# Kernel tuning notes

Measured on AMD Instinct MI355X. Metric: run time of the kernel, lower is better.

The kernel has to match this reference:

```python
import jax, jax.numpy as jnp
import numpy as np

HEADS = 8
DIM_HEAD = 64
QUERY_DIM = 512
CONTEXT_DIM = 768
INNER = HEADS * DIM_HEAD  # 512
SCALE = DIM_HEAD ** -0.5


def setup_inputs() -> dict:
    key = jax.random.key(0)
    ks = jax.random.split(key, 7)
    B, N, M = 4, 2048, 2048
    x = jax.random.normal(ks[0], (B, N, QUERY_DIM), dtype=jnp.float32)
    context = jax.random.normal(ks[1], (B, M, CONTEXT_DIM), dtype=jnp.float32)
    # torch Linear weights: [out_features, in_features], y = x @ W.T
    s = 0.02
    Wq = jax.random.normal(ks[2], (INNER, QUERY_DIM), dtype=jnp.float32) * s
    Wk = jax.random.normal(ks[3], (INNER, CONTEXT_DIM), dtype=jnp.float32) * s
    Wv = jax.random.normal(ks[4], (INNER, CONTEXT_DIM), dtype=jnp.float32) * s
    Wo = jax.random.normal(ks[5], (QUERY_DIM, INNER), dtype=jnp.float32) * s
    bo = jax.random.normal(ks[6], (QUERY_DIM,), dtype=jnp.float32) * s
    return {"x": x, "context": context, "Wq": Wq, "Wk": Wk, "Wv": Wv, "Wo": Wo, "bo": bo}


def reference(x, context, Wq, Wk, Wv, Wo, bo):
    b, n, _ = x.shape
    m = context.shape[1]
    h, d = HEADS, DIM_HEAD
    # Projections (bias=False for q/k/v)
    q = jnp.einsum('bnc,ec->bne', x, Wq)        # [b, n, inner]
    k = jnp.einsum('bmc,ec->bme', context, Wk)  # [b, m, inner]
    v = jnp.einsum('bmc,ec->bme', context, Wv)
    # Split heads
    q = q.reshape(b, n, h, d)
    k = k.reshape(b, m, h, d)
    v = v.reshape(b, m, h, d)
    # Scores in fp32 (original casts q,k to float), scaled by dim_head**-0.5
    sim = jnp.einsum('bihd,bjhd->bhij', q.astype(jnp.float32), k.astype(jnp.float32)) * SCALE
    attn = jax.nn.softmax(sim, axis=-1).astype(v.dtype)
    out = jnp.einsum('bhij,bjhd->bihd', attn, v).reshape(b, n, h * d)
    # Output projection with bias (dropout=0 -> identity)
    return jnp.einsum('bne,oe->bno', out, Wo) + bo
```

## Files before the change

kernel.cpp:

```cpp
#include <hip/hip_runtime.h>
#include <hip/hip_bf16.h>
#include <math.h>


typedef __bf16 bf16x8 __attribute__((ext_vector_type(8)));
typedef __bf16 bf16x4 __attribute__((ext_vector_type(4)));
typedef short s16x4 __attribute__((ext_vector_type(4)));
typedef float f32x4 __attribute__((ext_vector_type(4)));

#define QSCALE 0.18033688011112042f

__device__ __forceinline__ f32x4 mfma32(bf16x8 a, bf16x8 b, f32x4 c) {
  return __builtin_amdgcn_mfma_f32_16x16x32_bf16(a, b, c, 0, 0, 0);
}
__device__ __forceinline__ f32x4 mfma16(s16x4 a, s16x4 b, f32x4 c) {
  return __builtin_amdgcn_mfma_f32_16x16x16bf16_1k(a, b, c, 0, 0, 0);
}

__global__ __launch_bounds__(256) void cast_all(
    const float* __restrict__ x, const float* __restrict__ ctx,
    const float* __restrict__ wq, const float* __restrict__ wk,
    const float* __restrict__ wv, const float* __restrict__ wo,
    __bf16* __restrict__ xb, __bf16* __restrict__ cb,
    __bf16* __restrict__ wqb, __bf16* __restrict__ wkb,
    __bf16* __restrict__ wvb, __bf16* __restrict__ wob) {
  const int B0 = 1048576;
  const int B1 = 2621440;
  const int B2 = 2686976;
  const int B3 = 2785280;
  const int B4 = 2883584;
  const int B5 = 2949120;
  for (int i = blockIdx.x * blockDim.x + threadIdx.x; i < B5;
       i += gridDim.x * blockDim.x) {
    const float* s;
    __bf16* d;
    int off;
    if (i < B0)      { s = x;   d = xb;  off = i; }
    else if (i < B1) { s = ctx; d = cb;  off = i - B0; }
    else if (i < B2) { s = wq;  d = wqb; off = i - B1; }
    else if (i < B3) { s = wk;  d = wkb; off = i - B2; }
    else if (i < B4) { s = wv;  d = wvb; off = i - B3; }
    else             { s = wo;  d = wob; off = i - B4; }
    float4 f = ((const float4*)s)[off];
    union { __bf16 b[4]; ushort4 u; } cv;
    cv.b[0] = (__bf16)f.x; cv.b[1] = (__bf16)f.y;
    cv.b[2] = (__bf16)f.z; cv.b[3] = (__bf16)f.w;
    ((ushort4*)d)[off] = cv.u;
  }
}

template <int MODE>
__device__ __forceinline__ void gemm_body(
    const __bf16* __restrict__ A, const __bf16* __restrict__ B,
    __bf16* __restrict__ Cout, int Kd, float scale, int m0, int n0,
    __bf16 (*As)[40], __bf16 (*Bs)[40]) {
  const int t = threadIdx.x;
  const int w = t >> 6;
  const int lane = t & 63;
  const int ln = lane & 15;
  const int qd = lane >> 4;
  const int wm = (w >> 1) * 64;
  const int wn = (w & 1) * 64;

  f32x4 zero4 = {0.f, 0.f, 0.f, 0.f};
  f32x4 acc[4][4];
#pragma unroll
  for (int i = 0; i < 4; ++i)
#pragma unroll
    for (int j = 0; j < 4; ++j) acc[i][j] = zero4;

  const int r = t >> 1;
  const int c0 = (t & 1) * 16;
  const __bf16* gA = A + (size_t)(m0 + r) * Kd + c0;
  const __bf16* gB = B + (size_t)(n0 + r) * Kd + c0;

  for (int kc = 0; kc < Kd; kc += 32) {
    uint4 a0 = *(const uint4*)(gA + kc);
    uint4 a1 = *(const uint4*)(gA + kc + 8);
    uint4 b0 = *(const uint4*)(gB + kc);
    uint4 b1 = *(const uint4*)(gB + kc + 8);
    __syncthreads();
    *(uint4*)&As[r][c0] = a0;
    *(uint4*)&As[r][c0 + 8] = a1;
    *(uint4*)&Bs[r][c0] = b0;
    *(uint4*)&Bs[r][c0 + 8] = b1;
    __syncthreads();
    bf16x8 af[4], bfr[4];
#pragma unroll
    for (int i = 0; i < 4; ++i) {
      af[i] = *(const bf16x8*)&As[wm + i * 16 + ln][qd * 8];
      bfr[i] = *(const bf16x8*)&Bs[wn + i * 16 + ln][qd * 8];
    }
#pragma unroll
    for (int i = 0; i < 4; ++i)
#pragma unroll
      for (int j = 0; j < 4; ++j) {
        if (MODE == 1)
          acc[i][j] = mfma32(af[i], bfr[j], acc[i][j]);
        else
          acc[i][j] = mfma32(bfr[j], af[i], acc[i][j]);
      }
  }

#pragma unroll
  for (int i = 0; i < 4; ++i)
#pragma unroll
    for (int j = 0; j < 4; ++j) {
      if (MODE == 0) {
        const int gm = m0 + wm + i * 16 + ln;
        const int gn0 = n0 + wn + j * 16 + qd * 4;
        const int bb = gm >> 11, tok = gm & 2047;
        const int hh = gn0 >> 6, dd0 = gn0 & 63;
        bf16x4 v;
#pragma unroll
        for (int rg = 0; rg < 4; ++rg) v[rg] = (__bf16)(acc[i][j][rg] * scale);
        *(bf16x4*)(Cout + (((size_t)bb * 8 + hh) * 2048 + tok) * 64 + dd0) = v;
      } else {
        const int gm0 = m0 + wm + i * 16 + qd * 4;
        const int gn = n0 + wn + j * 16 + ln;
        const int bb = gm0 >> 11;
        const int tokbase = (gm0 & 2047) & ~31;
        const int up = qd * 8 + (i & 1) * 4;
        const int hh = gn >> 6, dd = gn & 63;
        bf16x4 v;
#pragma unroll
        for (int rg = 0; rg < 4; ++rg) v[rg] = (__bf16)acc[i][j][rg];
        *(bf16x4*)(Cout + (((size_t)bb * 8 + hh) * 64 + dd) * 2048 + tokbase +
                   up) = v;
      }
    }
}

__global__ __launch_bounds__(256, 3) void proj_qkv(
    const __bf16* __restrict__ xb, const __bf16* __restrict__ cb,
    const __bf16* __restrict__ Wq, const __bf16* __restrict__ Wk,
    const __bf16* __restrict__ Wv, __bf16* __restrict__ Qw,
    __bf16* __restrict__ Kw, __bf16* __restrict__ Vtw) {
  __shared__ __bf16 As[128][40];
  __shared__ __bf16 Bs[128][40];
  const int m0 = blockIdx.x * 128;
  const int job = blockIdx.y >> 2;
  const int n0 = (blockIdx.y & 3) * 128;
  if (job == 0)
    gemm_body<0>(xb, Wq, Qw, 512, QSCALE, m0, n0, As, Bs);
  else if (job == 1)
    gemm_body<0>(cb, Wk, Kw, 768, 1.0f, m0, n0, As, Bs);
  else
    gemm_body<1>(cb, Wv, Vtw, 768, 1.0f, m0, n0, As, Bs);
}

__global__ __launch_bounds__(256) void gemm_out(
    const __bf16* __restrict__ O0, const __bf16* __restrict__ O1,
    const float* __restrict__ lbuf,
    const __bf16* __restrict__ B,
    float* __restrict__ C, const float* __restrict__ bias) {
  const int m0 = blockIdx.x * 64;
  const int n0 = blockIdx.y * 128;
  const int t = threadIdx.x;
  const int w = t >> 6;
  const int lane = t & 63;
  const int ln = lane & 15;
  const int qd = lane >> 4;
  const int wm = (w >> 1) * 32;
  const int wn = (w & 1) * 64;

  __shared__ __bf16 As[64][40];
  __shared__ __bf16 Bs[128][40];

  f32x4 zero4 = {0.f, 0.f, 0.f, 0.f};
  f32x4 acc[2][4];
#pragma unroll
  for (int i = 0; i < 2; ++i)
#pragma unroll
    for (int j = 0; j < 4; ++j) acc[i][j] = zero4;

  const int ra = t >> 2, ca = (t & 3) * 8;
  const int rb = t >> 1, cb = (t & 1) * 16;
  const int gm_s = m0 + ra;
  const int bidx = gm_s >> 11, tok_s = gm_s & 2047;
  const size_t aoff = (size_t)gm_s * 512 + ca;
  const __bf16* gB = B + (size_t)(n0 + rb) * 512 + cb;

  float inv[8];
#pragma unroll
  for (int hh = 0; hh < 8; ++hh) {
    const float l0 = lbuf[((size_t)bidx * 8 + hh) * 2048 + tok_s];
    const float l1 = lbuf[65536 + ((size_t)bidx * 8 + hh) * 2048 + tok_s];
    inv[hh] = 1.0f / (l0 + l1);
  }

#pragma unroll
  for (int kc = 0; kc < 512; kc += 32) {
    const float iv = inv[kc >> 6];
    union { bf16x8 v; uint4 u; } u0, u1, rr;
    u0.u = *(const uint4*)(O0 + aoff + kc);
    u1.u = *(const uint4*)(O1 + aoff + kc);
    uint4 b0 = *(const uint4*)(gB + kc);
    uint4 b1 = *(const uint4*)(gB + kc + 8);
#pragma unroll
    for (int e = 0; e < 8; ++e)
      rr.v[e] = (__bf16)(((float)u0.v[e] + (float)u1.v[e]) * iv);
    __syncthreads();
    *(uint4*)&As[ra][ca] = rr.u;
    *(uint4*)&Bs[rb][cb] = b0;
    *(uint4*)&Bs[rb][cb + 8] = b1;
    __syncthreads();
    bf16x8 af[2], bfr[4];
#pragma unroll
    for (int i = 0; i < 2; ++i)
      af[i] = *(const bf16x8*)&As[wm + i * 16 + ln][qd * 8];
#pragma unroll
    for (int j = 0; j < 4; ++j)
      bfr[j] = *(const bf16x8*)&Bs[wn + j * 16 + ln][qd * 8];
#pragma unroll
    for (int i = 0; i < 2; ++i)
#pragma unroll
      for (int j = 0; j < 4; ++j)
        acc[i][j] = mfma32(bfr[j], af[i], acc[i][j]);
  }

#pragma unroll
  for (int i = 0; i < 2; ++i)
#pragma unroll
    for (int j = 0; j < 4; ++j) {
      const int gm = m0 + wm + i * 16 + ln;
      const int gn0 = n0 + wn + j * 16 + qd * 4;
      f32x4 bi = *(const f32x4*)&bias[gn0];
      f32x4 v = acc[i][j] + bi;
      *(f32x4*)&C[(size_t)gm * 512 + gn0] = v;
    }
}

__global__ __launch_bounds__(256, 4) void attn_kernel(
    const __bf16* __restrict__ Q,
    const __bf16* __restrict__ K,
    const __bf16* __restrict__ Vt,
    __bf16* __restrict__ Oh,
    float* __restrict__ lbuf) {
  const int S = 2048;
  const int qt = blockIdx.x;
  const int bh = blockIdx.y;
  const int sp = blockIdx.z;
  const int b = bh >> 3, h = bh & 7;
  const int t = threadIdx.x;
  const int w = t >> 6;
  const int lane = t & 63;
  const int ln = lane & 15;
  const int qd = lane >> 4;

  __shared__ __align__(16) __bf16 Ks[128][72];
  __shared__ __align__(16) __bf16 Vts[64][136];

  bf16x8 bq[2][2];
  {
    const __bf16* qb =
        Q + ((size_t)bh * S + qt * 128 + w * 32 + ln) * 64 + qd * 8;
#pragma unroll
    for (int mt = 0; mt < 2; ++mt)
#pragma unroll
      for (int kst = 0; kst < 2; ++kst)
        bq[mt][kst] = *(const bf16x8*)(qb + mt * 1024 + kst * 32);
  }

  f32x4 zero4 = {0.f, 0.f, 0.f, 0.f};
  f32x4 o[2][4];
#pragma unroll
  for (int mt = 0; mt < 2; ++mt)
#pragma unroll
    for (int i = 0; i < 4; ++i) o[mt][i] = zero4;
  float lrow[2] = {0.f, 0.f};

  const int kr = t >> 1, kc = (t & 1) * 32;
  const int vd = t >> 2, vc = (t & 3) * 32;
  const int kt0 = sp * 8;

  for (int kt = kt0; kt < kt0 + 8; ++kt) {
    const uint4* gK =
        (const uint4*)(K + ((size_t)bh * S + kt * 128 + kr) * 64 + kc);
    const uint4* gV =
        (const uint4*)(Vt + ((size_t)bh * 64 + vd) * S + kt * 128 + vc);
    uint4 kv0 = gK[0], kv1 = gK[1], kv2 = gK[2], kv3 = gK[3];
    uint4 vv0 = gV[0], vv1 = gV[1], vv2 = gV[2], vv3 = gV[3];
    __syncthreads();
    {
      uint4* dK = (uint4*)&Ks[kr][kc];
      dK[0] = kv0; dK[1] = kv1; dK[2] = kv2; dK[3] = kv3;
      uint4* dV = (uint4*)&Vts[vd][vc];
      dV[0] = vv0; dV[1] = vv1; dV[2] = vv2; dV[3] = vv3;
    }
    __syncthreads();

#pragma unroll
    for (int c = 0; c < 4; ++c) {
      bf16x8 av[4];
#pragma unroll
      for (int i = 0; i < 4; ++i)
        av[i] = *(const bf16x8*)&Vts[i * 16 + ln][c * 32 + qd * 8];

      f32x4 s[2][2];
      s[0][0] = zero4; s[0][1] = zero4; s[1][0] = zero4; s[1][1] = zero4;
#pragma unroll
      for (int e = 0; e < 2; ++e) {
        const int nt = c * 2 + e;
#pragma unroll
        for (int kst = 0; kst < 2; ++kst) {
          bf16x8 ak = *(const bf16x8*)&Ks[nt * 16 + ln][kst * 32 + qd * 8];
          s[e][0] = mfma32(ak, bq[0][kst], s[e][0]);
          s[e][1] = mfma32(ak, bq[1][kst], s[e][1]);
        }
      }
#pragma unroll
      for (int e = 0; e < 2; ++e)
#pragma unroll
        for (int mt = 0; mt < 2; ++mt) {
          float rs = 0.f;
#pragma unroll
          for (int rg = 0; rg < 4; ++rg) {
            float p = exp2f(s[e][mt][rg]);
            s[e][mt][rg] = p;
            rs += p;
          }
          lrow[mt] += rs;
        }
#pragma unroll
      for (int e = 0; e < 2; ++e) {
        bf16x4 c0, c1;
#pragma unroll
        for (int rg = 0; rg < 4; ++rg) {
          c0[rg] = (__bf16)s[e][0][rg];
          c1[rg] = (__bf16)s[e][1][rg];
        }
        s16x4 p0 = __builtin_bit_cast(s16x4, c0);
        s16x4 p1 = __builtin_bit_cast(s16x4, c1);
#pragma unroll
        for (int i = 0; i < 4; ++i) {
          union { bf16x8 v; bf16x4 hh[2]; } U;
          U.v = av[i];
          s16x4 a = __builtin_bit_cast(s16x4, U.hh[e]);
          o[0][i] = mfma16(a, p0, o[0][i]);
          o[1][i] = mfma16(a, p1, o[1][i]);
        }
      }
    }
  }

  __bf16* Osp = Oh + (size_t)sp * 8192 * 512;
#pragma unroll
  for (int mt = 0; mt < 2; ++mt) {
    float l = lrow[mt];
    l += __shfl_xor(l, 16);
    l += __shfl_xor(l, 32);
    const int tok = qt * 128 + w * 32 + mt * 16 + ln;
    if (qd == 0) lbuf[((size_t)sp * 32 + bh) * 2048 + tok] = l;
#pragma unroll
    for (int i = 0; i < 4; ++i) {
      bf16x4 v;
#pragma unroll
      for (int rg = 0; rg < 4; ++rg) v[rg] = (__bf16)o[mt][i][rg];
      const int col = h * 64 + i * 16 + qd * 4;
      *(bf16x4*)&Osp[((size_t)b * S + tok) * 512 + col] = v;
    }
  }
}

extern "C" void kernel_launch(void* const* d_in, const int* in_sizes, int n_in,
                              void* d_out, int out_size, void* d_ws,
                              size_t ws_size, hipStream_t stream) {
  const float* x = (const float*)d_in[0];
  const float* ctx = (const float*)d_in[1];
  const float* Wq = (const float*)d_in[2];
  const float* Wk = (const float*)d_in[3];
  const float* Wv = (const float*)d_in[4];
  const float* Wo = (const float*)d_in[5];
  const float* bo = (const float*)d_in[6];

  char* p = (char*)d_ws;
  __bf16* xb = (__bf16*)p;   p += (size_t)8192 * 512 * 2;
  __bf16* cb = (__bf16*)p;   p += (size_t)8192 * 768 * 2;
  __bf16* wqb = (__bf16*)p;  p += (size_t)512 * 512 * 2;
  __bf16* wkb = (__bf16*)p;  p += (size_t)512 * 768 * 2;
  __bf16* wvb = (__bf16*)p;  p += (size_t)512 * 768 * 2;
  __bf16* wob = (__bf16*)p;  p += (size_t)512 * 512 * 2;
  __bf16* Qw = (__bf16*)p;   p += (size_t)8192 * 512 * 2;
  __bf16* Kw = (__bf16*)p;   p += (size_t)8192 * 512 * 2;
  __bf16* Vtw = (__bf16*)p;  p += (size_t)8192 * 512 * 2;
  __bf16* Oh = (__bf16*)p;   p += (size_t)2 * 8192 * 512 * 2;
  float* lbuf = (float*)p;   p += (size_t)2 * 32 * 2048 * 4;

  cast_all<<<2880, 256, 0, stream>>>(x, ctx, Wq, Wk, Wv, Wo, xb, cb, wqb, wkb,
                                     wvb, wob);

  dim3 gp(64, 12);
  proj_qkv<<<gp, 256, 0, stream>>>(xb, cb, wqb, wkb, wvb, Qw, Kw, Vtw);

  dim3 ga(16, 32, 2);
  attn_kernel<<<ga, 256, 0, stream>>>(Qw, Kw, Vtw, Oh, lbuf);

  dim3 go(128, 4);
  gemm_out<<<go, 256, 0, stream>>>(Oh, Oh + (size_t)8192 * 512, lbuf, wob,
                                   (float*)d_out, bo);
}
```

Measured before the change: 206.4 us.

## Double-buffer GEMMs with direct global-to-LDS loads and compute row sums via MFMA

The projection and output GEMMs switch to global_load_lds direct copies into a double-buffered, k-chunk-major shared layout, dropping one barrier per k step and overlapping the next tile's load with MFMA work. The output GEMM also prefetches and normalises the next A tile in registers. The attention kernel computes softmax row sums with an extra MFMA against a ones vector instead of VALU adds and shuffles, and uses the raw exp2 builtin. The V^T layout is changed to plain token order with a new LDS pitch and narrower reads. Risks include LDS bank conflicts in the unpadded layout and async-load ordering relying on a single barrier.

```diff
diff --git a/kernel.cpp b/kernel.cpp
--- a/kernel.cpp
+++ b/kernel.cpp
@@ -10,11 +10,23 @@
 
 #define QSCALE 0.18033688011112042f
 
+#if __has_builtin(__builtin_amdgcn_exp2f)
+#define EXP2(x) __builtin_amdgcn_exp2f(x)
+#else
+#define EXP2(x) exp2f(x)
+#endif
+
 __device__ __forceinline__ f32x4 mfma32(bf16x8 a, bf16x8 b, f32x4 c) {
   return __builtin_amdgcn_mfma_f32_16x16x32_bf16(a, b, c, 0, 0, 0);
 }
 __device__ __forceinline__ f32x4 mfma16(s16x4 a, s16x4 b, f32x4 c) {
   return __builtin_amdgcn_mfma_f32_16x16x16bf16_1k(a, b, c, 0, 0, 0);
+}
+
+__device__ __forceinline__ void glds16(const void* g, void* l) {
+  __builtin_amdgcn_global_load_lds(
+      (const __attribute__((address_space(1))) unsigned int*)g,
+      (__attribute__((address_space(3))) unsigned int*)l, 16, 0, 0);
 }
 
 __global__ __launch_bounds__(256) void cast_all(
@@ -53,7 +65,7 @@
 __device__ __forceinline__ void gemm_body(
     const __bf16* __restrict__ A, const __bf16* __restrict__ B,
     __bf16* __restrict__ Cout, int Kd, float scale, int m0, int n0,
-    __bf16 (*As)[40], __bf16 (*Bs)[40]) {
+    __bf16 (*As)[4][128][8], __bf16 (*Bs)[4][128][8]) {
   const int t = threadIdx.x;
   const int w = t >> 6;
   const int lane = t & 63;
@@ -69,27 +81,30 @@
 #pragma unroll
     for (int j = 0; j < 4; ++j) acc[i][j] = zero4;
 
-  const int r = t >> 1;
-  const int c0 = (t & 1) * 16;
-  const __bf16* gA = A + (size_t)(m0 + r) * Kd + c0;
-  const __bf16* gB = B + (size_t)(n0 + r) * Kd + c0;
-
+  const __bf16* gA0 = A + (size_t)(m0 + lane) * Kd + w * 8;
+  const __bf16* gA1 = A + (size_t)(m0 + 64 + lane) * Kd + w * 8;
+  const __bf16* gB0 = B + (size_t)(n0 + lane) * Kd + w * 8;
+  const __bf16* gB1 = B + (size_t)(n0 + 64 + lane) * Kd + w * 8;
+
+  glds16(gA0, &As[0][w][0][0]);
+  glds16(gA1, &As[0][w][64][0]);
+  glds16(gB0, &Bs[0][w][0][0]);
+  glds16(gB1, &Bs[0][w][64][0]);
+
+  int buf = 0;
   for (int kc = 0; kc < Kd; kc += 32) {
-    uint4 a0 = *(const uint4*)(gA + kc);
-    uint4 a1 = *(const uint4*)(gA + kc + 8);
-    uint4 b0 = *(const uint4*)(gB + kc);
-    uint4 b1 = *(const uint4*)(gB + kc + 8);
     __syncthreads();
-    *(uint4*)&As[r][c0] = a0;
-    *(uint4*)&As[r][c0 + 8] = a1;
-    *(uint4*)&Bs[r][c0] = b0;
-    *(uint4*)&Bs[r][c0 + 8] = b1;
-    __syncthreads();
+    if (kc + 32 < Kd) {
+      glds16(gA0 + kc + 32, &As[buf ^ 1][w][0][0]);
+      glds16(gA1 + kc + 32, &As[buf ^ 1][w][64][0]);
+      glds16(gB0 + kc + 32, &Bs[buf ^ 1][w][0][0]);
+      glds16(gB1 + kc + 32, &Bs[buf ^ 1][w][64][0]);
+    }
     bf16x8 af[4], bfr[4];
 #pragma unroll
     for (int i = 0; i < 4; ++i) {
-      af[i] = *(const bf16x8*)&As[wm + i * 16 + ln][qd * 8];
-      bfr[i] = *(const bf16x8*)&Bs[wn + i * 16 + ln][qd * 8];
+      af[i] = *(const bf16x8*)&As[buf][qd][wm + i * 16 + ln][0];
+      bfr[i] = *(const bf16x8*)&Bs[buf][qd][wn + i * 16 + ln][0];
     }
 #pragma unroll
     for (int i = 0; i < 4; ++i)
@@ -100,6 +115,7 @@
         else
           acc[i][j] = mfma32(bfr[j], af[i], acc[i][j]);
       }
+    buf ^= 1;
   }
 
 #pragma unroll
@@ -118,15 +134,12 @@
       } else {
         const int gm0 = m0 + wm + i * 16 + qd * 4;
         const int gn = n0 + wn + j * 16 + ln;
-        const int bb = gm0 >> 11;
-        const int tokbase = (gm0 & 2047) & ~31;
-        const int up = qd * 8 + (i & 1) * 4;
+        const int bb = gm0 >> 11, tok0 = gm0 & 2047;
         const int hh = gn >> 6, dd = gn & 63;
         bf16x4 v;
 #pragma unroll
         for (int rg = 0; rg < 4; ++rg) v[rg] = (__bf16)acc[i][j][rg];
-        *(bf16x4*)(Cout + (((size_t)bb * 8 + hh) * 64 + dd) * 2048 + tokbase +
-                   up) = v;
+        *(bf16x4*)(Cout + (((size_t)bb * 8 + hh) * 64 + dd) * 2048 + tok0) = v;
       }
     }
 }
@@ -136,8 +149,8 @@
     const __bf16* __restrict__ Wq, const __bf16* __restrict__ Wk,
     const __bf16* __restrict__ Wv, __bf16* __restrict__ Qw,
     __bf16* __restrict__ Kw, __bf16* __restrict__ Vtw) {
-  __shared__ __bf16 As[128][40];
-  __shared__ __bf16 Bs[128][40];
+  __shared__ __align__(16) __bf16 As[2][4][128][8];
+  __shared__ __align__(16) __bf16 Bs[2][4][128][8];
   const int m0 = blockIdx.x * 128;
   const int job = blockIdx.y >> 2;
   const int n0 = (blockIdx.y & 3) * 128;
@@ -164,8 +177,8 @@
   const int wm = (w >> 1) * 32;
   const int wn = (w & 1) * 64;
 
-  __shared__ __bf16 As[64][40];
-  __shared__ __bf16 Bs[128][40];
+  __shared__ __align__(16) __bf16 As[2][64][40];
+  __shared__ __align__(16) __bf16 Bs[2][4][128][8];
 
   f32x4 zero4 = {0.f, 0.f, 0.f, 0.f};
   f32x4 acc[2][4];
@@ -175,11 +188,11 @@
     for (int j = 0; j < 4; ++j) acc[i][j] = zero4;
 
   const int ra = t >> 2, ca = (t & 3) * 8;
-  const int rb = t >> 1, cb = (t & 1) * 16;
   const int gm_s = m0 + ra;
   const int bidx = gm_s >> 11, tok_s = gm_s & 2047;
   const size_t aoff = (size_t)gm_s * 512 + ca;
-  const __bf16* gB = B + (size_t)(n0 + rb) * 512 + cb;
+  const __bf16* gB0 = B + (size_t)(n0 + lane) * 512 + w * 8;
+  const __bf16* gB1 = B + (size_t)(n0 + 64 + lane) * 512 + w * 8;
 
   float inv[8];
 #pragma unroll
@@ -189,34 +202,53 @@
     inv[hh] = 1.0f / (l0 + l1);
   }
 
-#pragma unroll
-  for (int kc = 0; kc < 512; kc += 32) {
-    const float iv = inv[kc >> 6];
+  {
     union { bf16x8 v; uint4 u; } u0, u1, rr;
-    u0.u = *(const uint4*)(O0 + aoff + kc);
-    u1.u = *(const uint4*)(O1 + aoff + kc);
-    uint4 b0 = *(const uint4*)(gB + kc);
-    uint4 b1 = *(const uint4*)(gB + kc + 8);
+    u0.u = *(const uint4*)(O0 + aoff);
+    u1.u = *(const uint4*)(O1 + aoff);
+    glds16(gB0, &Bs[0][w][0][0]);
+    glds16(gB1, &Bs[0][w][64][0]);
+    const float iv = inv[0];
 #pragma unroll
     for (int e = 0; e < 8; ++e)
       rr.v[e] = (__bf16)(((float)u0.v[e] + (float)u1.v[e]) * iv);
+    *(uint4*)&As[0][ra][ca] = rr.u;
+  }
+
+  int buf = 0;
+#pragma unroll
+  for (int k = 0; k < 16; ++k) {
     __syncthreads();
-    *(uint4*)&As[ra][ca] = rr.u;
-    *(uint4*)&Bs[rb][cb] = b0;
-    *(uint4*)&Bs[rb][cb + 8] = b1;
-    __syncthreads();
+    uint4 o0n, o1n;
+    if (k < 15) {
+      o0n = *(const uint4*)(O0 + aoff + (k + 1) * 32);
+      o1n = *(const uint4*)(O1 + aoff + (k + 1) * 32);
+      glds16(gB0 + (k + 1) * 32, &Bs[buf ^ 1][w][0][0]);
+      glds16(gB1 + (k + 1) * 32, &Bs[buf ^ 1][w][64][0]);
+    }
     bf16x8 af[2], bfr[4];
 #pragma unroll
     for (int i = 0; i < 2; ++i)
-      af[i] = *(const bf16x8*)&As[wm + i * 16 + ln][qd * 8];
+      af[i] = *(const bf16x8*)&As[buf][wm + i * 16 + ln][qd * 8];
 #pragma unroll
     for (int j = 0; j < 4; ++j)
-      bfr[j] = *(const bf16x8*)&Bs[wn + j * 16 + ln][qd * 8];
+      bfr[j] = *(const bf16x8*)&Bs[buf][qd][wn + j * 16 + ln][0];
 #pragma unroll
     for (int i = 0; i < 2; ++i)
 #pragma unroll
       for (int j = 0; j < 4; ++j)
         acc[i][j] = mfma32(bfr[j], af[i], acc[i][j]);
+    if (k < 15) {
+      union { bf16x8 v; uint4 u; } u0, u1, rr;
+      u0.u = o0n;
+      u1.u = o1n;
+      const float iv = inv[(k + 1) >> 1];
+#pragma unroll
+      for (int e = 0; e < 8; ++e)
+        rr.v[e] = (__bf16)(((float)u0.v[e] + (float)u1.v[e]) * iv);
+      *(uint4*)&As[buf ^ 1][ra][ca] = rr.u;
+    }
+    buf ^= 1;
   }
 
 #pragma unroll
@@ -249,7 +281,7 @@
   const int qd = lane >> 4;
 
   __shared__ __align__(16) __bf16 Ks[128][72];
-  __shared__ __align__(16) __bf16 Vts[64][136];
+  __shared__ __align__(16) __bf16 Vts[64][132];
 
   bf16x8 bq[2][2];
   {
@@ -264,11 +296,14 @@
 
   f32x4 zero4 = {0.f, 0.f, 0.f, 0.f};
   f32x4 o[2][4];
-#pragma unroll
-  for (int mt = 0; mt < 2; ++mt)
+  f32x4 o_l[2];
+#pragma unroll
+  for (int mt = 0; mt < 2; ++mt) {
 #pragma unroll
     for (int i = 0; i < 4; ++i) o[mt][i] = zero4;
-  float lrow[2] = {0.f, 0.f};
+    o_l[mt] = zero4;
+  }
+  const s16x4 ones = {0x3F80, 0x3F80, 0x3F80, 0x3F80};
 
   const int kr = t >> 1, kc = (t & 1) * 32;
   const int vd = t >> 2, vc = (t & 3) * 32;
@@ -285,18 +320,16 @@
     {
       uint4* dK = (uint4*)&Ks[kr][kc];
       dK[0] = kv0; dK[1] = kv1; dK[2] = kv2; dK[3] = kv3;
-      uint4* dV = (uint4*)&Vts[vd][vc];
-      dV[0] = vv0; dV[1] = vv1; dV[2] = vv2; dV[3] = vv3;
+      uint2* dV = (uint2*)&Vts[vd][vc];
+      dV[0] = *(uint2*)&vv0; dV[1] = *((uint2*)&vv0 + 1);
+      dV[2] = *(uint2*)&vv1; dV[3] = *((uint2*)&vv1 + 1);
+      dV[4] = *(uint2*)&vv2; dV[5] = *((uint2*)&vv2 + 1);
+      dV[6] = *(uint2*)&vv3; dV[7] = *((uint2*)&vv3 + 1);
     }
     __syncthreads();
 
 #pragma unroll
     for (int c = 0; c < 4; ++c) {
-      bf16x8 av[4];
-#pragma unroll
-      for (int i = 0; i < 4; ++i)
-        av[i] = *(const bf16x8*)&Vts[i * 16 + ln][c * 32 + qd * 8];
-
       f32x4 s[2][2];
       s[0][0] = zero4; s[0][1] = zero4; s[1][0] = zero4; s[1][1] = zero4;
 #pragma unroll
@@ -312,18 +345,12 @@
 #pragma unroll
       for (int e = 0; e < 2; ++e)
 #pragma unroll
-        for (int mt = 0; mt < 2; ++mt) {
-          float rs = 0.f;
-#pragma unroll
-          for (int rg = 0; rg < 4; ++rg) {
-            float p = exp2f(s[e][mt][rg]);
-            s[e][mt][rg] = p;
-            rs += p;
-          }
-          lrow[mt] += rs;
-        }
+        for (int mt = 0; mt < 2; ++mt)
+#pragma unroll
+          for (int rg = 0; rg < 4; ++rg) s[e][mt][rg] = EXP2(s[e][mt][rg]);
 #pragma unroll
       for (int e = 0; e < 2; ++e) {
+        const int nt = c * 2 + e;
         bf16x4 c0, c1;
 #pragma unroll
         for (int rg = 0; rg < 4; ++rg) {
@@ -332,11 +359,12 @@
         }
         s16x4 p0 = __builtin_bit_cast(s16x4, c0);
         s16x4 p1 = __builtin_bit_cast(s16x4, c1);
+        o_l[0] = mfma16(ones, p0, o_l[0]);
+        o_l[1] = mfma16(ones, p1, o_l[1]);
 #pragma unroll
         for (int i = 0; i < 4; ++i) {
-          union { bf16x8 v; bf16x4 hh[2]; } U;
-          U.v = av[i];
-          s16x4 a = __builtin_bit_cast(s16x4, U.hh[e]);
+          bf16x4 av = *(const bf16x4*)&Vts[i * 16 + ln][nt * 16 + qd * 4];
+          s16x4 a = __builtin_bit_cast(s16x4, av);
           o[0][i] = mfma16(a, p0, o[0][i]);
           o[1][i] = mfma16(a, p1, o[1][i]);
         }
@@ -347,11 +375,8 @@
   __bf16* Osp = Oh + (size_t)sp * 8192 * 512;
 #pragma unroll
   for (int mt = 0; mt < 2; ++mt) {
-    float l = lrow[mt];
-    l += __shfl_xor(l, 16);
-    l += __shfl_xor(l, 32);
     const int tok = qt * 128 + w * 32 + mt * 16 + ln;
-    if (qd == 0) lbuf[((size_t)sp * 32 + bh) * 2048 + tok] = l;
+    if (qd == 0) lbuf[((size_t)sp * 32 + bh) * 2048 + tok] = o_l[mt][0];
 #pragma unroll
     for (int i = 0; i < 4; ++i) {
       bf16x4 v;
```

New measurement: 204.0 us. About the same (-1.2%).

## Shrink GEMM tiles, compute softmax row sums via MFMA, change V layout

Applied to the files above, without the earlier changes.

The QKV projection tile drops from 128x128 to 64x128 and the output GEMM tile from 64x128 to 64x64, which doubles both grids and raises the occupancy hints so more blocks run at once. In the attention kernel, row sums of exp(P) are now accumulated with an extra MFMA against a ones vector rather than scalar adds plus shuffles. V^T is stored in natural token order, and V fragments are read from LDS per step as bf16x4 with a different padding. A raw exp2 builtin is also used. The smaller tiles give up operand reuse per block, and the extra MFMAs and LDS reads add work to the attention inner loop.

```diff
diff --git a/kernel.cpp b/kernel.cpp
--- a/kernel.cpp
+++ b/kernel.cpp
@@ -9,6 +9,12 @@
 typedef float f32x4 __attribute__((ext_vector_type(4)));
 
 #define QSCALE 0.18033688011112042f
+
+#if __has_builtin(__builtin_amdgcn_exp2f)
+#define EXP2(x) __builtin_amdgcn_exp2f(x)
+#else
+#define EXP2(x) exp2f(x)
+#endif
 
 __device__ __forceinline__ f32x4 mfma32(bf16x8 a, bf16x8 b, f32x4 c) {
   return __builtin_amdgcn_mfma_f32_16x16x32_bf16(a, b, c, 0, 0, 0);
@@ -50,7 +56,7 @@
 }
 
 template <int MODE>
-__device__ __forceinline__ void gemm_body(
+__device__ __forceinline__ void gemm_body64(
     const __bf16* __restrict__ A, const __bf16* __restrict__ B,
     __bf16* __restrict__ Cout, int Kd, float scale, int m0, int n0,
     __bf16 (*As)[40], __bf16 (*Bs)[40]) {
@@ -59,40 +65,39 @@
   const int lane = t & 63;
   const int ln = lane & 15;
   const int qd = lane >> 4;
-  const int wm = (w >> 1) * 64;
+  const int wm = (w >> 1) * 32;
   const int wn = (w & 1) * 64;
 
   f32x4 zero4 = {0.f, 0.f, 0.f, 0.f};
-  f32x4 acc[4][4];
-#pragma unroll
-  for (int i = 0; i < 4; ++i)
+  f32x4 acc[2][4];
+#pragma unroll
+  for (int i = 0; i < 2; ++i)
 #pragma unroll
     for (int j = 0; j < 4; ++j) acc[i][j] = zero4;
 
-  const int r = t >> 1;
-  const int c0 = (t & 1) * 16;
-  const __bf16* gA = A + (size_t)(m0 + r) * Kd + c0;
-  const __bf16* gB = B + (size_t)(n0 + r) * Kd + c0;
+  const int ra = t >> 2, ca = (t & 3) * 8;
+  const int rb = t >> 1, cbx = (t & 1) * 16;
+  const __bf16* gA = A + (size_t)(m0 + ra) * Kd + ca;
+  const __bf16* gB = B + (size_t)(n0 + rb) * Kd + cbx;
 
   for (int kc = 0; kc < Kd; kc += 32) {
     uint4 a0 = *(const uint4*)(gA + kc);
-    uint4 a1 = *(const uint4*)(gA + kc + 8);
     uint4 b0 = *(const uint4*)(gB + kc);
     uint4 b1 = *(const uint4*)(gB + kc + 8);
     __syncthreads();
-    *(uint4*)&As[r][c0] = a0;
-    *(uint4*)&As[r][c0 + 8] = a1;
-    *(uint4*)&Bs[r][c0] = b0;
-    *(uint4*)&Bs[r][c0 + 8] = b1;
-    __syncthreads();
-    bf16x8 af[4], bfr[4];
-#pragma unroll
-    for (int i = 0; i < 4; ++i) {
+    *(uint4*)&As[ra][ca] = a0;
+    *(uint4*)&Bs[rb][cbx] = b0;
+    *(uint4*)&Bs[rb][cbx + 8] = b1;
+    __syncthreads();
+    bf16x8 af[2], bfr[4];
+#pragma unroll
+    for (int i = 0; i < 2; ++i)
       af[i] = *(const bf16x8*)&As[wm + i * 16 + ln][qd * 8];
-      bfr[i] = *(const bf16x8*)&Bs[wn + i * 16 + ln][qd * 8];
-    }
-#pragma unroll
-    for (int i = 0; i < 4; ++i)
+#pragma unroll
+    for (int j = 0; j < 4; ++j)
+      bfr[j] = *(const bf16x8*)&Bs[wn + j * 16 + ln][qd * 8];
+#pragma unroll
+    for (int i = 0; i < 2; ++i)
 #pragma unroll
       for (int j = 0; j < 4; ++j) {
         if (MODE == 1)
@@ -103,7 +108,7 @@
   }
 
 #pragma unroll
-  for (int i = 0; i < 4; ++i)
+  for (int i = 0; i < 2; ++i)
 #pragma unroll
     for (int j = 0; j < 4; ++j) {
       if (MODE == 0) {
@@ -118,68 +123,64 @@
       } else {
         const int gm0 = m0 + wm + i * 16 + qd * 4;
         const int gn = n0 + wn + j * 16 + ln;
-        const int bb = gm0 >> 11;
-        const int tokbase = (gm0 & 2047) & ~31;
-        const int up = qd * 8 + (i & 1) * 4;
+        const int bb = gm0 >> 11, tok0 = gm0 & 2047;
         const int hh = gn >> 6, dd = gn & 63;
         bf16x4 v;
 #pragma unroll
         for (int rg = 0; rg < 4; ++rg) v[rg] = (__bf16)acc[i][j][rg];
-        *(bf16x4*)(Cout + (((size_t)bb * 8 + hh) * 64 + dd) * 2048 + tokbase +
-                   up) = v;
+        *(bf16x4*)(Cout + (((size_t)bb * 8 + hh) * 64 + dd) * 2048 + tok0) = v;
       }
     }
 }
 
-__global__ __launch_bounds__(256, 3) void proj_qkv(
+__global__ __launch_bounds__(256, 4) void proj_qkv(
     const __bf16* __restrict__ xb, const __bf16* __restrict__ cb,
     const __bf16* __restrict__ Wq, const __bf16* __restrict__ Wk,
     const __bf16* __restrict__ Wv, __bf16* __restrict__ Qw,
     __bf16* __restrict__ Kw, __bf16* __restrict__ Vtw) {
-  __shared__ __bf16 As[128][40];
+  __shared__ __bf16 As[64][40];
   __shared__ __bf16 Bs[128][40];
-  const int m0 = blockIdx.x * 128;
+  const int m0 = blockIdx.x * 64;
   const int job = blockIdx.y >> 2;
   const int n0 = (blockIdx.y & 3) * 128;
   if (job == 0)
-    gemm_body<0>(xb, Wq, Qw, 512, QSCALE, m0, n0, As, Bs);
+    gemm_body64<0>(xb, Wq, Qw, 512, QSCALE, m0, n0, As, Bs);
   else if (job == 1)
-    gemm_body<0>(cb, Wk, Kw, 768, 1.0f, m0, n0, As, Bs);
+    gemm_body64<0>(cb, Wk, Kw, 768, 1.0f, m0, n0, As, Bs);
   else
-    gemm_body<1>(cb, Wv, Vtw, 768, 1.0f, m0, n0, As, Bs);
-}
-
-__global__ __launch_bounds__(256) void gemm_out(
+    gemm_body64<1>(cb, Wv, Vtw, 768, 1.0f, m0, n0, As, Bs);
+}
+
+__global__ __launch_bounds__(256, 4) void gemm_out(
     const __bf16* __restrict__ O0, const __bf16* __restrict__ O1,
     const float* __restrict__ lbuf,
     const __bf16* __restrict__ B,
     float* __restrict__ C, const float* __restrict__ bias) {
   const int m0 = blockIdx.x * 64;
-  const int n0 = blockIdx.y * 128;
+  const int n0 = blockIdx.y * 64;
   const int t = threadIdx.x;
   const int w = t >> 6;
   const int lane = t & 63;
   const int ln = lane & 15;
   const int qd = lane >> 4;
   const int wm = (w >> 1) * 32;
-  const int wn = (w & 1) * 64;
+  const int wn = (w & 1) * 32;
 
   __shared__ __bf16 As[64][40];
-  __shared__ __bf16 Bs[128][40];
+  __shared__ __bf16 Bs[64][40];
 
   f32x4 zero4 = {0.f, 0.f, 0.f, 0.f};
-  f32x4 acc[2][4];
+  f32x4 acc[2][2];
 #pragma unroll
   for (int i = 0; i < 2; ++i)
 #pragma unroll
-    for (int j = 0; j < 4; ++j) acc[i][j] = zero4;
+    for (int j = 0; j < 2; ++j) acc[i][j] = zero4;
 
   const int ra = t >> 2, ca = (t & 3) * 8;
-  const int rb = t >> 1, cb = (t & 1) * 16;
   const int gm_s = m0 + ra;
   const int bidx = gm_s >> 11, tok_s = gm_s & 2047;
   const size_t aoff = (size_t)gm_s * 512 + ca;
-  const __bf16* gB = B + (size_t)(n0 + rb) * 512 + cb;
+  const __bf16* gB = B + (size_t)(n0 + ra) * 512 + ca;
 
   float inv[8];
 #pragma unroll
@@ -189,40 +190,37 @@
     inv[hh] = 1.0f / (l0 + l1);
   }
 
-#pragma unroll
   for (int kc = 0; kc < 512; kc += 32) {
     const float iv = inv[kc >> 6];
     union { bf16x8 v; uint4 u; } u0, u1, rr;
     u0.u = *(const uint4*)(O0 + aoff + kc);
     u1.u = *(const uint4*)(O1 + aoff + kc);
-    uint4 b0 = *(const uint4*)(gB + kc);
-    uint4 b1 = *(const uint4*)(gB + kc + 8);
+    uint4 bv = *(const uint4*)(gB + kc);
 #pragma unroll
     for (int e = 0; e < 8; ++e)
       rr.v[e] = (__bf16)(((float)u0.v[e] + (float)u1.v[e]) * iv);
     __syncthreads();
     *(uint4*)&As[ra][ca] = rr.u;
-    *(uint4*)&Bs[rb][cb] = b0;
-    *(uint4*)&Bs[rb][cb + 8] = b1;
-    __syncthreads();
-    bf16x8 af[2], bfr[4];
+    *(uint4*)&Bs[ra][ca] = bv;
+    __syncthreads();
+    bf16x8 af[2], bfr[2];
 #pragma unroll
     for (int i = 0; i < 2; ++i)
       af[i] = *(const bf16x8*)&As[wm + i * 16 + ln][qd * 8];
 #pragma unroll
-    for (int j = 0; j < 4; ++j)
+    for (int j = 0; j < 2; ++j)
       bfr[j] = *(const bf16x8*)&Bs[wn + j * 16 + ln][qd * 8];
 #pragma unroll
     for (int i = 0; i < 2; ++i)
 #pragma unroll
-      for (int j = 0; j < 4; ++j)
+      for (int j = 0; j < 2; ++j)
         acc[i][j] = mfma32(bfr[j], af[i], acc[i][j]);
   }
 
 #pragma unroll
   for (int i = 0; i < 2; ++i)
 #pragma unroll
-    for (int j = 0; j < 4; ++j) {
+    for (int j = 0; j < 2; ++j) {
       const int gm = m0 + wm + i * 16 + ln;
       const int gn0 = n0 + wn + j * 16 + qd * 4;
       f32x4 bi = *(const f32x4*)&bias[gn0];
@@ -249,7 +247,7 @@
   const int qd = lane >> 4;
 
   __shared__ __align__(16) __bf16 Ks[128][72];
-  __shared__ __align__(16) __bf16 Vts[64][136];
+  __shared__ __align__(16) __bf16 Vts[64][132];
 
   bf16x8 bq[2][2];
   {
@@ -264,11 +262,14 @@
 
   f32x4 zero4 = {0.f, 0.f, 0.f, 0.f};
   f32x4 o[2][4];
-#pragma unroll
-  for (int mt = 0; mt < 2; ++mt)
+  f32x4 o_l[2];
+#pragma unroll
+  for (int mt = 0; mt < 2; ++mt) {
 #pragma unroll
     for (int i = 0; i < 4; ++i) o[mt][i] = zero4;
-  float lrow[2] = {0.f, 0.f};
+    o_l[mt] = zero4;
+  }
+  const s16x4 ones = {0x3F80, 0x3F80, 0x3F80, 0x3F80};
 
   const int kr = t >> 1, kc = (t & 1) * 32;
   const int vd = t >> 2, vc = (t & 3) * 32;
@@ -285,18 +286,16 @@
     {
       uint4* dK = (uint4*)&Ks[kr][kc];
       dK[0] = kv0; dK[1] = kv1; dK[2] = kv2; dK[3] = kv3;
-      uint4* dV = (uint4*)&Vts[vd][vc];
-      dV[0] = vv0; dV[1] = vv1; dV[2] = vv2; dV[3] = vv3;
+      uint2* dV = (uint2*)&Vts[vd][vc];
+      dV[0] = *(uint2*)&vv0; dV[1] = *((uint2*)&vv0 + 1);
+      dV[2] = *(uint2*)&vv1; dV[3] = *((uint2*)&vv1 + 1);
+      dV[4] = *(uint2*)&vv2; dV[5] = *((uint2*)&vv2 + 1);
+      dV[6] = *(uint2*)&vv3; dV[7] = *((uint2*)&vv3 + 1);
     }
     __syncthreads();
 
 #pragma unroll
     for (int c = 0; c < 4; ++c) {
-      bf16x8 av[4];
-#pragma unroll
-      for (int i = 0; i < 4; ++i)
-        av[i] = *(const bf16x8*)&Vts[i * 16 + ln][c * 32 + qd * 8];
-
       f32x4 s[2][2];
       s[0][0] = zero4; s[0][1] = zero4; s[1][0] = zero4; s[1][1] = zero4;
 #pragma unroll
@@ -312,18 +311,12 @@
 #pragma unroll
       for (int e = 0; e < 2; ++e)
 #pragma unroll
-        for (int mt = 0; mt < 2; ++mt) {
-          float rs = 0.f;
-#pragma unroll
-          for (int rg = 0; rg < 4; ++rg) {
-            float p = exp2f(s[e][mt][rg]);
-            s[e][mt][rg] = p;
-            rs += p;
-          }
-          lrow[mt] += rs;
-        }
+        for (int mt = 0; mt < 2; ++mt)
+#pragma unroll
+          for (int rg = 0; rg < 4; ++rg) s[e][mt][rg] = EXP2(s[e][mt][rg]);
 #pragma unroll
       for (int e = 0; e < 2; ++e) {
+        const int nt = c * 2 + e;
         bf16x4 c0, c1;
 #pragma unroll
         for (int rg = 0; rg < 4; ++rg) {
@@ -332,11 +325,12 @@
         }
         s16x4 p0 = __builtin_bit_cast(s16x4, c0);
         s16x4 p1 = __builtin_bit_cast(s16x4, c1);
+        o_l[0] = mfma16(ones, p0, o_l[0]);
+        o_l[1] = mfma16(ones, p1, o_l[1]);
 #pragma unroll
         for (int i = 0; i < 4; ++i) {
-          union { bf16x8 v; bf16x4 hh[2]; } U;
-          U.v = av[i];
-          s16x4 a = __builtin_bit_cast(s16x4, U.hh[e]);
+          bf16x4 av = *(const bf16x4*)&Vts[i * 16 + ln][nt * 16 + qd * 4];
+          s16x4 a = __builtin_bit_cast(s16x4, av);
           o[0][i] = mfma16(a, p0, o[0][i]);
           o[1][i] = mfma16(a, p1, o[1][i]);
         }
@@ -347,11 +341,8 @@
   __bf16* Osp = Oh + (size_t)sp * 8192 * 512;
 #pragma unroll
   for (int mt = 0; mt < 2; ++mt) {
-    float l = lrow[mt];
-    l += __shfl_xor(l, 16);
-    l += __shfl_xor(l, 32);
     const int tok = qt * 128 + w * 32 + mt * 16 + ln;
-    if (qd == 0) lbuf[((size_t)sp * 32 + bh) * 2048 + tok] = l;
+    if (qd == 0) lbuf[((size_t)sp * 32 + bh) * 2048 + tok] = o_l[mt][0];
 #pragma unroll
     for (int i = 0; i < 4; ++i) {
       bf16x4 v;
@@ -390,13 +381,13 @@
   cast_all<<<2880, 256, 0, stream>>>(x, ctx, Wq, Wk, Wv, Wo, xb, cb, wqb, wkb,
                                      wvb, wob);
 
-  dim3 gp(64, 12);
+  dim3 gp(128, 12);
   proj_qkv<<<gp, 256, 0, stream>>>(xb, cb, wqb, wkb, wvb, Qw, Kw, Vtw);
 
   dim3 ga(16, 32, 2);
   attn_kernel<<<ga, 256, 0, stream>>>(Qw, Kw, Vtw, Oh, lbuf);
 
-  dim3 go(128, 4);
+  dim3 go(128, 8);
   gemm_out<<<go, 256, 0, stream>>>(Oh, Oh + (size_t)8192 * 512, lbuf, wob,
                                    (float*)d_out, bo);
 }
```

Measured after the change: 202.6 us. About the same (-1.8%).
